# Kernel tuning notes

Hardware: AMD Instinct MI355X
Metric: run time of the kernel (lower is better)

## Reference

```python
import jax, jax.numpy as jnp
import numpy as np

HEADS = 12
EPS = 1e-12  # torch F.normalize eps


def _l2_normalize(x, axis):
    norm = jnp.sqrt(jnp.sum(x * x, axis=axis, keepdims=True))
    return x / jnp.maximum(norm, EPS)


def setup_inputs() -> dict:
    key = jax.random.key(0)
    k1, k2, k3 = jax.random.split(key, 3)
    B, N, D = 8, 4096, 768
    x = jax.random.normal(k1, (B, N, D), dtype=jnp.float32)
    Wqkv = jax.random.normal(k2, (D, 3 * D), dtype=jnp.float32) * (1.0 / np.sqrt(D))
    temperature = jnp.ones((1, HEADS, 1, 1), dtype=jnp.float32)
    Wout = jax.random.normal(k3, (D, D), dtype=jnp.float32) * (1.0 / np.sqrt(D))
    bout = jnp.zeros((D,), dtype=jnp.float32)
    return {"x": x, "Wqkv": Wqkv, "temperature": temperature, "Wout": Wout, "bout": bout}


def reference(x, Wqkv, temperature, Wout, bout):
    B, N, D = x.shape
    H = HEADS
    d = D // H
    qkv = x @ Wqkv  # (B, N, 3D)
    q, k, v = jnp.split(qkv, 3, axis=-1)
    # b n (h d) -> b h n d
    def to_bhnd(t):
        return t.reshape(B, N, H, d).transpose(0, 2, 1, 3)
    q = to_bhnd(q)
    k = to_bhnd(k)
    v = to_bhnd(v)
    # q: normalize over token axis (torch: q is bhnd, dim=-2 -> n)
    q = _l2_normalize(q, axis=2)
    # k: torch layout is bhdn, normalized over dim=-1 (n); in bhnd that's axis=2
    k = _l2_normalize(k, axis=2) * temperature  # (1,H,1,1) broadcasts over bhnd
    # attention[p, q_idx] = sum_n k[n, p] * q[n, q_idx]  -> (B, H, d, d)
    attn = jnp.einsum('bhnp,bhnq->bhpq', k, q)
    attn = jax.nn.softmax(attn, axis=-1)
    # out[n, q_idx] = sum_p v[n, p] * attn[p, q_idx]
    out = jnp.einsum('bhnp,bhpq->bhnq', v, attn)
    # b h n d -> b n (h d)
    out = out.transpose(0, 2, 1, 3).reshape(B, N, D)
    return out @ Wout + bout
```

## Files before the change

### kernel.cpp

```cpp
#include <hip/hip_runtime.h>

typedef __attribute__((ext_vector_type(8))) short short8;
typedef __attribute__((ext_vector_type(4))) float f32x4;

__device__ __forceinline__ float b2f(unsigned short u) {
    unsigned int i = ((unsigned int)u) << 16;
    return __builtin_bit_cast(float, i);
}
__device__ __forceinline__ unsigned short f2b(float f) {
    unsigned int u = __builtin_bit_cast(unsigned int, f);
    unsigned int r = (u + 0x7fffu + ((u >> 16) & 1u)) >> 16;
    return (unsigned short)r;
}

__device__ __forceinline__ void async16(unsigned short* lds, const unsigned short* g) {
    __builtin_amdgcn_global_load_lds(
        (const __attribute__((address_space(1))) unsigned int*)g,
        (__attribute__((address_space(3))) unsigned int*)lds,
        16, 0, 0);
}

__device__ __forceinline__ void xcd_swizzle(int& bx, int& by) {
    if ((gridDim.y & 7) == 0) {
        const int nx = gridDim.x;
        const int rows_per_xcd = gridDim.y >> 3;
        const int flat = blockIdx.y * nx + blockIdx.x;
        const int xcd = flat & 7;
        const int i = flat >> 3;
        by = xcd * rows_per_xcd + i / nx;
        bx = i % nx;
    } else {
        bx = blockIdx.x; by = blockIdx.y;
    }
}

__global__ __launch_bounds__(256)
void cvt_f32_bf16(const float* __restrict__ in, unsigned short* __restrict__ out,
                  long long n8) {
    const long long i = ((long long)blockIdx.x * 256 + threadIdx.x) * 8;
    if (i >= n8) return;
    f32x4 a = *(const f32x4*)(in + i);
    f32x4 b = *(const f32x4*)(in + i + 4);
    short8 o;
    #pragma unroll
    for (int j = 0; j < 4; ++j) { o[j] = (short)f2b(a[j]); o[j + 4] = (short)f2b(b[j]); }
    *(short8*)(out + i) = o;
}

__global__ __launch_bounds__(256)
void transpose_f32_bf16(const float* __restrict__ in, unsigned short* __restrict__ out,
                        int R, int C) {
    __shared__ unsigned short t[32][33];
    const int r0 = blockIdx.y * 32, c0 = blockIdx.x * 32;
    const int tx = threadIdx.x & 31, ty = threadIdx.x >> 5;
    #pragma unroll
    for (int i = 0; i < 32; i += 8)
        t[ty + i][tx] = f2b(in[(size_t)(r0 + ty + i) * C + c0 + tx]);
    __syncthreads();
    #pragma unroll
    for (int i = 0; i < 32; i += 8)
        out[(size_t)(c0 + ty + i) * R + r0 + tx] = t[tx][ty + i];
}

__global__ __launch_bounds__(256)
void cvt_tr64(const float* __restrict__ in, unsigned short* __restrict__ rm,
              unsigned short* __restrict__ tm) {
    __shared__ unsigned short T[64][72];
    const int c0 = blockIdx.x * 64, r0 = blockIdx.y * 64;
    const int tr = threadIdx.x >> 2, tc = (threadIdx.x & 3) * 16;
    {
        const float* src = in + (size_t)(r0 + tr) * 768 + c0 + tc;
        f32x4 a0 = *(const f32x4*)(src);
        f32x4 a1 = *(const f32x4*)(src + 4);
        f32x4 a2 = *(const f32x4*)(src + 8);
        f32x4 a3 = *(const f32x4*)(src + 12);
        short8 o0, o1;
        #pragma unroll
        for (int j = 0; j < 4; ++j) {
            o0[j] = (short)f2b(a0[j]); o0[j + 4] = (short)f2b(a1[j]);
            o1[j] = (short)f2b(a2[j]); o1[j + 4] = (short)f2b(a3[j]);
        }
        *(short8*)&T[tr][tc] = o0;
        *(short8*)&T[tr][tc + 8] = o1;
        unsigned short* d = rm + (size_t)(r0 + tr) * 768 + c0 + tc;
        *(short8*)(d) = o0;
        *(short8*)(d + 8) = o1;
    }
    __syncthreads();
    short8 s0, s1;
    #pragma unroll
    for (int e = 0; e < 8; ++e) {
        s0[e] = (short)T[tc + e][tr];
        s1[e] = (short)T[tc + 8 + e][tr];
    }
    unsigned short* d = tm + (size_t)(c0 + tr) * 32768 + r0 + tc;
    *(short8*)(d) = s0;
    *(short8*)(d + 8) = s1;
}

__global__ __launch_bounds__(256, 2)
void gram_split(const unsigned short* __restrict__ xT, unsigned short* __restrict__ Gp) {
    __shared__ unsigned short As[128 * 32];
    __shared__ unsigned short Bs[128 * 32];
    const int z = blockIdx.z, b = z >> 2, s = z & 3;
    const int tid  = threadIdx.x;
    const int wave = tid >> 6, lane = tid & 63;
    const int quad = lane >> 4, m16 = lane & 15;
    const int bm = blockIdx.y * 128, bn = blockIdx.x * 128;
    const int wm = (wave >> 1) * 64, wn = (wave & 1) * 64;
    const int srow = wave * 32 + (lane >> 2);
    const int scol = (lane & 3) * 8;
    const unsigned short* base = xT + (size_t)b * 4096 + s * 1024 + scol;
    const unsigned short* Ag = base + (size_t)(bm + srow) * 32768;
    const unsigned short* Bg = base + (size_t)(bn + srow) * 32768;
    unsigned short* Asw = &As[(wave * 32) * 32];
    unsigned short* Bsw = &Bs[(wave * 32) * 32];
    f32x4 acc[4][4] = {};

    for (int k0 = 0; k0 < 1024; k0 += 32) {
        __syncthreads();
        async16(Asw,           Ag + k0);
        async16(Asw + 16 * 32, Ag + k0 + (size_t)16 * 32768);
        async16(Bsw,           Bg + k0);
        async16(Bsw + 16 * 32, Bg + k0 + (size_t)16 * 32768);
        __syncthreads();
        short8 af[4], bfr[4];
        #pragma unroll
        for (int i = 0; i < 4; ++i)
            af[i] = *(const short8*)&As[(wm + i * 16 + m16) * 32 + quad * 8];
        #pragma unroll
        for (int j = 0; j < 4; ++j)
            bfr[j] = *(const short8*)&Bs[(wn + j * 16 + m16) * 32 + quad * 8];
        #pragma unroll
        for (int i = 0; i < 4; ++i)
            #pragma unroll
            for (int j = 0; j < 4; ++j)
                acc[i][j] = __builtin_amdgcn_mfma_f32_16x16x32_bf16(af[i], bfr[j], acc[i][j], 0, 0, 0);
    }
    unsigned short* C = Gp + (size_t)z * 589824;
    #pragma unroll
    for (int j = 0; j < 4; ++j) {
        const int col = bn + wn + j * 16 + m16;
        #pragma unroll
        for (int i = 0; i < 4; ++i)
            #pragma unroll
            for (int r = 0; r < 4; ++r) {
                const int row = bm + wm + i * 16 + quad * 4 + r;
                C[(size_t)row * 768 + col] = f2b(acc[i][j][r]);
            }
    }
}

__global__ __launch_bounds__(256)
void g_reduce(const unsigned short* __restrict__ Gp, unsigned short* __restrict__ G) {
    const int b = blockIdx.y;
    const int off = blockIdx.x * 2048 + threadIdx.x * 8;
    const unsigned short* p = Gp + (size_t)b * 4 * 589824 + off;
    float s[8] = {};
    #pragma unroll
    for (int sp = 0; sp < 4; ++sp) {
        short8 v = *(const short8*)(p + (size_t)sp * 589824);
        #pragma unroll
        for (int e = 0; e < 8; ++e) s[e] += b2f((unsigned short)v[e]);
    }
    short8 o;
    #pragma unroll
    for (int e = 0; e < 8; ++e) o[e] = (short)f2b(s[e]);
    *(short8*)(G + (size_t)b * 589824 + off) = o;
}

template<int OM>
__global__ __launch_bounds__(256, 2)
void gemm_bt_g(const unsigned short* A, const unsigned short* BT,
               void* __restrict__ Cv, const float* __restrict__ bias,
               int K, int lda, int ldb, int ldc,
               long long sA, long long sB, long long sC) {
    __shared__ unsigned short As[128 * 32];
    __shared__ unsigned short Bs[128 * 32];
    const int z = blockIdx.z;
    A  += (size_t)z * sA;
    BT += (size_t)z * sB;
    int bxi, byi;
    xcd_swizzle(bxi, byi);
    const int tid  = threadIdx.x;
    const int wave = tid >> 6, lane = tid & 63;
    const int quad = lane >> 4, m16 = lane & 15;
    const int bm = byi * 128, bn = bxi * 128;
    const int wm = (wave >> 1) * 64, wn = (wave & 1) * 64;
    const int srow = wave * 32 + (lane >> 2);
    const int scol = (lane & 3) * 8;
    const unsigned short* Ag = A + (size_t)(bm + srow) * lda + scol;
    const unsigned short* Bg = BT + (size_t)(bn + srow) * ldb + scol;
    unsigned short* Asw = &As[(wave * 32) * 32];
    unsigned short* Bsw = &Bs[(wave * 32) * 32];
    f32x4 acc[4][4] = {};

    for (int k0 = 0; k0 < K; k0 += 32) {
        __syncthreads();
        async16(Asw,           Ag + k0);
        async16(Asw + 16 * 32, Ag + k0 + (size_t)16 * lda);
        async16(Bsw,           Bg + k0);
        async16(Bsw + 16 * 32, Bg + k0 + (size_t)16 * ldb);
        __syncthreads();
        short8 af[4], bfr[4];
        #pragma unroll
        for (int i = 0; i < 4; ++i)
            af[i] = *(const short8*)&As[(wm + i * 16 + m16) * 32 + quad * 8];
        #pragma unroll
        for (int j = 0; j < 4; ++j)
            bfr[j] = *(const short8*)&Bs[(wn + j * 16 + m16) * 32 + quad * 8];
        #pragma unroll
        for (int i = 0; i < 4; ++i)
            #pragma unroll
            for (int j = 0; j < 4; ++j)
                acc[i][j] = __builtin_amdgcn_mfma_f32_16x16x32_bf16(af[i], bfr[j], acc[i][j], 0, 0, 0);
    }

    if constexpr (OM == 0) {
        unsigned short* C = (unsigned short*)Cv + (size_t)z * sC;
        #pragma unroll
        for (int j = 0; j < 4; ++j) {
            const int col = bn + wn + j * 16 + m16;
            #pragma unroll
            for (int i = 0; i < 4; ++i)
                #pragma unroll
                for (int r = 0; r < 4; ++r) {
                    const int row = bm + wm + i * 16 + quad * 4 + r;
                    C[(size_t)row * ldc + col] = f2b(acc[i][j][r]);
                }
        }
    } else {
        float* C = (float*)Cv + (size_t)z * sC;
        #pragma unroll
        for (int j = 0; j < 4; ++j) {
            const int col = bn + wn + j * 16 + m16;
            const float bv = bias[col];
            #pragma unroll
            for (int i = 0; i < 4; ++i)
                #pragma unroll
                for (int r = 0; r < 4; ++r) {
                    const int row = bm + wm + i * 16 + quad * 4 + r;
                    C[(size_t)row * ldc + col] = acc[i][j][r] + bv;
                }
        }
    }
}

__global__ __launch_bounds__(256)
void rownorm(const unsigned short* __restrict__ W, const unsigned short* __restrict__ T,
             float* __restrict__ qn2, float* __restrict__ kn2) {
    const int row = blockIdx.x * 4 + (threadIdx.x >> 6);
    const int lane = threadIdx.x & 63;
    const int b = row / 1536, j = row % 1536;
    const unsigned short* wr = W + (size_t)j * 768;
    const unsigned short* tr = T + (size_t)b * 1179648 + (size_t)j * 768;
    float s = 0.f;
    {
        short8 a = *(const short8*)(wr + lane * 8);
        short8 c = *(const short8*)(tr + lane * 8);
        #pragma unroll
        for (int e = 0; e < 8; ++e) s += b2f((unsigned short)a[e]) * b2f((unsigned short)c[e]);
    }
    if (lane < 32) {
        short8 a = *(const short8*)(wr + 512 + lane * 8);
        short8 c = *(const short8*)(tr + 512 + lane * 8);
        #pragma unroll
        for (int e = 0; e < 8; ++e) s += b2f((unsigned short)a[e]) * b2f((unsigned short)c[e]);
    }
    #pragma unroll
    for (int o = 32; o; o >>= 1) s += __shfl_down(s, o);
    if (lane == 0) {
        if (j < 768) qn2[b * 768 + j] = s;
        else         kn2[b * 768 + j - 768] = s;
    }
}

__global__ __launch_bounds__(256)
void head_fused(const unsigned short* __restrict__ WqkvT,
                const unsigned short* __restrict__ TQKT,
                const unsigned short* __restrict__ Wbf,
                const float* __restrict__ qn2, const float* __restrict__ kn2,
                const float* __restrict__ temp, unsigned short* __restrict__ W2) {
    const int bh = blockIdx.x, b = bh / 12, h = bh % 12;
    __shared__ unsigned short As[64][72], Bs[64][72], At[64][72];
    __shared__ float Sf[64][65];
    __shared__ float qinv[64], kinv[64], red[64][4], red2[64][4];
    const int tid = threadIdx.x;
    const int wave = tid >> 6, lane = tid & 63;
    const int quad = lane >> 4, m16 = lane & 15;
    const int wr = wave >> 1, wc = wave & 1;

    if (tid < 64) {
        qinv[tid] = 1.0f / fmaxf(sqrtf(qn2[b * 768 + h * 64 + tid]), 1e-12f);
        kinv[tid] = 1.0f / fmaxf(sqrtf(kn2[b * 768 + h * 64 + tid]), 1e-12f);
    }

    f32x4 sacc[2][2] = {};
    const int srow = tid >> 3, scol8 = (tid & 7) * 8;
    const unsigned short* Arow = WqkvT + (size_t)(768 + h * 64) * 768;
    const unsigned short* Brow = TQKT + (size_t)(b * 1536 + h * 64) * 768;
    for (int k0 = 0; k0 < 768; k0 += 64) {
        __syncthreads();
        *(short8*)&As[srow][scol8]      = *(const short8*)(Arow + (size_t)srow * 768 + k0 + scol8);
        *(short8*)&As[srow + 32][scol8] = *(const short8*)(Arow + (size_t)(srow + 32) * 768 + k0 + scol8);
        *(short8*)&Bs[srow][scol8]      = *(const short8*)(Brow + (size_t)srow * 768 + k0 + scol8);
        *(short8*)&Bs[srow + 32][scol8] = *(const short8*)(Brow + (size_t)(srow + 32) * 768 + k0 + scol8);
        __syncthreads();
        #pragma unroll
        for (int ks = 0; ks < 2; ++ks) {
            short8 af[2], bv[2];
            af[0] = *(const short8*)&As[wr * 32 + m16][ks * 32 + quad * 8];
            af[1] = *(const short8*)&As[wr * 32 + 16 + m16][ks * 32 + quad * 8];
            bv[0] = *(const short8*)&Bs[wc * 32 + m16][ks * 32 + quad * 8];
            bv[1] = *(const short8*)&Bs[wc * 32 + 16 + m16][ks * 32 + quad * 8];
            #pragma unroll
            for (int i = 0; i < 2; ++i)
                #pragma unroll
                for (int j = 0; j < 2; ++j)
                    sacc[i][j] = __builtin_amdgcn_mfma_f32_16x16x32_bf16(af[i], bv[j], sacc[i][j], 0, 0, 0);
        }
    }
    __syncthreads();
    #pragma unroll
    for (int i = 0; i < 2; ++i)
        #pragma unroll
        for (int j = 0; j < 2; ++j)
            #pragma unroll
            for (int r = 0; r < 4; ++r)
                Sf[wr * 32 + i * 16 + quad * 4 + r][wc * 32 + j * 16 + m16] = sacc[i][j][r];
    __syncthreads();

    const float tt = temp[h];
    const int p = tid & 63, g = tid >> 6;
    float l[16], mx = -1e30f;
    const float kvp = tt * kinv[p];
    #pragma unroll
    for (int e = 0; e < 16; ++e) {
        l[e] = kvp * Sf[p][g * 16 + e] * qinv[g * 16 + e];
        mx = fmaxf(mx, l[e]);
    }
    red[p][g] = mx;
    __syncthreads();
    mx = fmaxf(fmaxf(red[p][0], red[p][1]), fmaxf(red[p][2], red[p][3]));
    float sum = 0.f;
    #pragma unroll
    for (int e = 0; e < 16; ++e) { l[e] = __expf(l[e] - mx); sum += l[e]; }
    red2[p][g] = sum;
    __syncthreads();
    sum = red2[p][0] + red2[p][1] + red2[p][2] + red2[p][3];
    const float inv = 1.0f / sum;
    #pragma unroll
    for (int e = 0; e < 16; ++e) At[g * 16 + e][p] = f2b(l[e] * inv);
    __syncthreads();

    const unsigned short* Wv = Wbf + 1536 + h * 64;
    unsigned short* W2b = W2 + (size_t)b * 589824 + h * 64;
    #pragma unroll
    for (int pass = 0; pass < 3; ++pass) {
        const int rb = wave * 192 + pass * 64;
        f32x4 wacc[4][4] = {};
        #pragma unroll
        for (int ks = 0; ks < 2; ++ks) {
            short8 av[4], bv[4];
            #pragma unroll
            for (int i = 0; i < 4; ++i)
                av[i] = *(const short8*)(Wv + (size_t)(rb + i * 16 + m16) * 2304 + ks * 32 + quad * 8);
            #pragma unroll
            for (int j = 0; j < 4; ++j)
                bv[j] = *(const short8*)&At[j * 16 + m16][ks * 32 + quad * 8];
            #pragma unroll
            for (int i = 0; i < 4; ++i)
                #pragma unroll
                for (int j = 0; j < 4; ++j)
                    wacc[i][j] = __builtin_amdgcn_mfma_f32_16x16x32_bf16(av[i], bv[j], wacc[i][j], 0, 0, 0);
        }
        #pragma unroll
        for (int j = 0; j < 4; ++j)
            #pragma unroll
            for (int i = 0; i < 4; ++i)
                #pragma unroll
                for (int r = 0; r < 4; ++r)
                    W2b[(size_t)(rb + i * 16 + quad * 4 + r) * 768 + j * 16 + m16] = f2b(wacc[i][j][r]);
    }
}

extern "C" void kernel_launch(void* const* d_in, const int* in_sizes, int n_in,
                              void* d_out, int out_size, void* d_ws, size_t ws_size,
                              hipStream_t stream) {
    const float *x = nullptr, *Wqkv = nullptr, *temp = nullptr, *Wout = nullptr, *bout = nullptr;
    for (int i = 0; i < n_in; ++i) {
        switch (in_sizes[i]) {
            case 25165824: x    = (const float*)d_in[i]; break;
            case 1769472:  Wqkv = (const float*)d_in[i]; break;
            case 12:       temp = (const float*)d_in[i]; break;
            case 589824:   Wout = (const float*)d_in[i]; break;
            case 768:      bout = (const float*)d_in[i]; break;
        }
    }
    float* out = (float*)d_out;

    char* ws = (char*)d_ws;
    unsigned short* WqkvT = (unsigned short*)(ws + 0);
    unsigned short* WoutT = (unsigned short*)(ws + 3538944);
    unsigned short* Wbf   = (unsigned short*)(ws + 4718592);
    unsigned short* xb    = (unsigned short*)(ws + 8257536);
    unsigned short* xT    = (unsigned short*)(ws + 58589184);
    unsigned short* G     = (unsigned short*)(ws + 58589184);
    unsigned short* TQKT  = (unsigned short*)(ws + 68026368);
    float*          qn2   = (float*)         (ws + 86900736);
    float*          kn2   = (float*)         (ws + 86925312);
    unsigned short* W2    = (unsigned short*)(ws + 86949888);
    unsigned short* FT    = (unsigned short*)(ws + 96387072);
    unsigned short* Gp    = (unsigned short*)(ws + 108920832);
    (void)ws_size;

    transpose_f32_bf16<<<dim3(72, 24), 256, 0, stream>>>(Wqkv, WqkvT, 768, 2304);
    transpose_f32_bf16<<<dim3(24, 24), 256, 0, stream>>>(Wout, WoutT, 768, 768);
    cvt_f32_bf16<<<dim3(864), 256, 0, stream>>>(Wqkv, Wbf, 1769472LL);

    cvt_tr64<<<dim3(12, 512), 256, 0, stream>>>(x, xb, xT);

    gram_split<<<dim3(6, 6, 32), 256, 0, stream>>>(xT, Gp);
    g_reduce<<<dim3(288, 8), 256, 0, stream>>>(Gp, G);

    gemm_bt_g<0><<<dim3(6, 12, 8), 256, 0, stream>>>(
        WqkvT, G, TQKT, nullptr, 768, 768, 768, 768, 0LL, 589824LL, 1179648LL);

    rownorm<<<dim3(3072), 256, 0, stream>>>(WqkvT, TQKT, qn2, kn2);

    head_fused<<<dim3(96), 256, 0, stream>>>(WqkvT, TQKT, Wbf, qn2, kn2, temp, W2);

    gemm_bt_g<0><<<dim3(6, 6, 8), 256, 0, stream>>>(
        WoutT, W2, FT, nullptr, 768, 768, 768, 768, 0LL, 589824LL, 589824LL);

    gemm_bt_g<2><<<dim3(6, 32, 8), 256, 0, stream>>>(
        xb, FT, out, bout, 768, 768, 768, 768, 3145728LL, 589824LL, 3145728LL);
}
```

Before: 424.0 us.

## Exploit Gram symmetry with upper-triangle tiles and deeper split-K

The Gram matrix x^T x is now computed only for the 21 upper-triangular 128x128 tiles instead of all 36. Split-K goes from 4 to 8 slices, and a new reduce kernel sums the partials and mirrors off-diagonal tiles through a shared-memory transpose. The two weight-prep kernels for Wqkv are merged so the row-major bf16 copy is written during the transpose pass. Launch bounds are raised to 4 blocks per CU for the GEMMs. The aim is to cut Gram FLOPs and launch count, at the cost of more partial traffic and a reduce grid of only 168 blocks.

```diff
diff --git a/kernel.cpp b/kernel.cpp
--- a/kernel.cpp
+++ b/kernel.cpp
@@ -35,31 +35,21 @@
 }
 
 __global__ __launch_bounds__(256)
-void cvt_f32_bf16(const float* __restrict__ in, unsigned short* __restrict__ out,
-                  long long n8) {
-    const long long i = ((long long)blockIdx.x * 256 + threadIdx.x) * 8;
-    if (i >= n8) return;
-    f32x4 a = *(const f32x4*)(in + i);
-    f32x4 b = *(const f32x4*)(in + i + 4);
-    short8 o;
-    #pragma unroll
-    for (int j = 0; j < 4; ++j) { o[j] = (short)f2b(a[j]); o[j + 4] = (short)f2b(b[j]); }
-    *(short8*)(out + i) = o;
-}
-
-__global__ __launch_bounds__(256)
-void transpose_f32_bf16(const float* __restrict__ in, unsigned short* __restrict__ out,
-                        int R, int C) {
+void wprep(const float* __restrict__ in, unsigned short* __restrict__ outT,
+           unsigned short* __restrict__ rm, int R, int C) {
     __shared__ unsigned short t[32][33];
     const int r0 = blockIdx.y * 32, c0 = blockIdx.x * 32;
     const int tx = threadIdx.x & 31, ty = threadIdx.x >> 5;
     #pragma unroll
+    for (int i = 0; i < 32; i += 8) {
+        unsigned short v = f2b(in[(size_t)(r0 + ty + i) * C + c0 + tx]);
+        t[ty + i][tx] = v;
+        if (rm) rm[(size_t)(r0 + ty + i) * C + c0 + tx] = v;
+    }
+    __syncthreads();
+    #pragma unroll
     for (int i = 0; i < 32; i += 8)
-        t[ty + i][tx] = f2b(in[(size_t)(r0 + ty + i) * C + c0 + tx]);
-    __syncthreads();
-    #pragma unroll
-    for (int i = 0; i < 32; i += 8)
-        out[(size_t)(c0 + ty + i) * R + r0 + tx] = t[tx][ty + i];
+        outT[(size_t)(c0 + ty + i) * R + r0 + tx] = t[tx][ty + i];
 }
 
 __global__ __launch_bounds__(256)
@@ -98,26 +88,35 @@
     *(short8*)(d + 8) = s1;
 }
 
-__global__ __launch_bounds__(256, 2)
-void gram_split(const unsigned short* __restrict__ xT, unsigned short* __restrict__ Gp) {
+__device__ __forceinline__ void tri_rc(int t, int& r, int& c) {
+    r = 0;
+    int rem = t;
+    while (rem >= 6 - r) { rem -= 6 - r; ++r; }
+    c = r + rem;
+}
+
+__global__ __launch_bounds__(256, 4)
+void gram_split_sym(const unsigned short* __restrict__ xT, unsigned short* __restrict__ Gp) {
     __shared__ unsigned short As[128 * 32];
     __shared__ unsigned short Bs[128 * 32];
-    const int z = blockIdx.z, b = z >> 2, s = z & 3;
+    const int z = blockIdx.y, b = z >> 3, s = z & 7;
+    int tr_, tc_;
+    tri_rc(blockIdx.x, tr_, tc_);
     const int tid  = threadIdx.x;
     const int wave = tid >> 6, lane = tid & 63;
     const int quad = lane >> 4, m16 = lane & 15;
-    const int bm = blockIdx.y * 128, bn = blockIdx.x * 128;
+    const int bm = tr_ * 128, bn = tc_ * 128;
     const int wm = (wave >> 1) * 64, wn = (wave & 1) * 64;
     const int srow = wave * 32 + (lane >> 2);
     const int scol = (lane & 3) * 8;
-    const unsigned short* base = xT + (size_t)b * 4096 + s * 1024 + scol;
+    const unsigned short* base = xT + (size_t)b * 4096 + s * 512 + scol;
     const unsigned short* Ag = base + (size_t)(bm + srow) * 32768;
     const unsigned short* Bg = base + (size_t)(bn + srow) * 32768;
     unsigned short* Asw = &As[(wave * 32) * 32];
     unsigned short* Bsw = &Bs[(wave * 32) * 32];
     f32x4 acc[4][4] = {};
 
-    for (int k0 = 0; k0 < 1024; k0 += 32) {
+    for (int k0 = 0; k0 < 512; k0 += 32) {
         __syncthreads();
         async16(Asw,           Ag + k0);
         async16(Asw + 16 * 32, Ag + k0 + (size_t)16 * 32768);
@@ -137,40 +136,61 @@
             for (int j = 0; j < 4; ++j)
                 acc[i][j] = __builtin_amdgcn_mfma_f32_16x16x32_bf16(af[i], bfr[j], acc[i][j], 0, 0, 0);
     }
-    unsigned short* C = Gp + (size_t)z * 589824;
+    unsigned short* C = Gp + ((size_t)z * 21 + blockIdx.x) * 16384;
     #pragma unroll
     for (int j = 0; j < 4; ++j) {
-        const int col = bn + wn + j * 16 + m16;
+        const int col = wn + j * 16 + m16;
         #pragma unroll
         for (int i = 0; i < 4; ++i)
             #pragma unroll
             for (int r = 0; r < 4; ++r) {
-                const int row = bm + wm + i * 16 + quad * 4 + r;
-                C[(size_t)row * 768 + col] = f2b(acc[i][j][r]);
+                const int row = wm + i * 16 + quad * 4 + r;
+                C[row * 128 + col] = f2b(acc[i][j][r]);
             }
     }
 }
 
 __global__ __launch_bounds__(256)
-void g_reduce(const unsigned short* __restrict__ Gp, unsigned short* __restrict__ G) {
-    const int b = blockIdx.y;
-    const int off = blockIdx.x * 2048 + threadIdx.x * 8;
-    const unsigned short* p = Gp + (size_t)b * 4 * 589824 + off;
-    float s[8] = {};
-    #pragma unroll
-    for (int sp = 0; sp < 4; ++sp) {
-        short8 v = *(const short8*)(p + (size_t)sp * 589824);
-        #pragma unroll
-        for (int e = 0; e < 8; ++e) s[e] += b2f((unsigned short)v[e]);
-    }
-    short8 o;
-    #pragma unroll
-    for (int e = 0; e < 8; ++e) o[e] = (short)f2b(s[e]);
-    *(short8*)(G + (size_t)b * 589824 + off) = o;
+void g_reduce_sym(const unsigned short* __restrict__ Gp, unsigned short* __restrict__ G) {
+    const int t = blockIdx.x, b = blockIdx.y;
+    int r, c;
+    tri_rc(t, r, c);
+    __shared__ unsigned short T[128][136];
+    const int tid = threadIdx.x;
+    const int row = tid >> 1, colbase = (tid & 1) * 64;
+    unsigned short* Gb = G + (size_t)b * 589824;
+    const unsigned short* p0 = Gp + ((size_t)(b * 8) * 21 + t) * 16384 + row * 128;
+    #pragma unroll
+    for (int k = 0; k < 8; ++k) {
+        const int col = colbase + k * 8;
+        float sum[8] = {};
+        #pragma unroll
+        for (int s = 0; s < 8; ++s) {
+            short8 v = *(const short8*)(p0 + (size_t)s * 21 * 16384 + col);
+            #pragma unroll
+            for (int e = 0; e < 8; ++e) sum[e] += b2f((unsigned short)v[e]);
+        }
+        short8 o;
+        #pragma unroll
+        for (int e = 0; e < 8; ++e) o[e] = (short)f2b(sum[e]);
+        *(short8*)&Gb[(size_t)(r * 128 + row) * 768 + c * 128 + col] = o;
+        *(short8*)&T[row][col] = o;
+    }
+    if (r != c) {
+        __syncthreads();
+        #pragma unroll
+        for (int k = 0; k < 8; ++k) {
+            const int col = colbase + k * 8;
+            short8 m;
+            #pragma unroll
+            for (int e = 0; e < 8; ++e) m[e] = (short)T[col + e][row];
+            *(short8*)&Gb[(size_t)(c * 128 + row) * 768 + r * 128 + col] = m;
+        }
+    }
 }
 
 template<int OM>
-__global__ __launch_bounds__(256, 2)
+__global__ __launch_bounds__(256, 4)
 void gemm_bt_g(const unsigned short* A, const unsigned short* BT,
                void* __restrict__ Cv, const float* __restrict__ bias,
                int K, int lda, int ldb, int ldc,
@@ -414,14 +434,13 @@
     unsigned short* Gp    = (unsigned short*)(ws + 108920832);
     (void)ws_size;
 
-    transpose_f32_bf16<<<dim3(72, 24), 256, 0, stream>>>(Wqkv, WqkvT, 768, 2304);
-    transpose_f32_bf16<<<dim3(24, 24), 256, 0, stream>>>(Wout, WoutT, 768, 768);
-    cvt_f32_bf16<<<dim3(864), 256, 0, stream>>>(Wqkv, Wbf, 1769472LL);
+    wprep<<<dim3(72, 24), 256, 0, stream>>>(Wqkv, WqkvT, Wbf, 768, 2304);
+    wprep<<<dim3(24, 24), 256, 0, stream>>>(Wout, WoutT, nullptr, 768, 768);
 
     cvt_tr64<<<dim3(12, 512), 256, 0, stream>>>(x, xb, xT);
 
-    gram_split<<<dim3(6, 6, 32), 256, 0, stream>>>(xT, Gp);
-    g_reduce<<<dim3(288, 8), 256, 0, stream>>>(Gp, G);
+    gram_split_sym<<<dim3(21, 64), 256, 0, stream>>>(xT, Gp);
+    g_reduce_sym<<<dim3(21, 8), 256, 0, stream>>>(Gp, G);
 
     gemm_bt_g<0><<<dim3(6, 12, 8), 256, 0, stream>>>(
         WqkvT, G, TQKT, nullptr, 768, 768, 768, 768, 0LL, 589824LL, 1179648LL);
```

Result: slower. 438.4 us (+3.4%).
